# Optimization experiments

Measured on AMD Instinct MI355X. Metric: run time of the kernel, lower is better.

## Reference

```python
import jax, jax.numpy as jnp
import numpy as np
from jax import lax

NEG_INF = -1e30  # finite stand-in for -inf (keeps grads clean)
BLANK = 6624


def setup_inputs() -> dict:
    key = jax.random.key(0)
    k1, k2 = jax.random.split(key)
    B, T, C, L = 32, 512, 6625, 32
    log_probs = jax.random.normal(k1, (B, T, C), dtype=jnp.float32)
    targets = jax.random.randint(k2, (B, L), 0, BLANK, dtype=jnp.int32)  # labels exclude blank
    input_lengths = jnp.full((B,), T, dtype=jnp.int32)
    target_lengths = jnp.full((B,), L, dtype=jnp.int32)
    return {"log_probs": log_probs, "targets": targets,
            "input_lengths": input_lengths, "target_lengths": target_lengths}


def _ctc_loss(lp, targets, input_lengths, target_lengths, blank):
    # lp: [B, T, C] (already log-normalized as in the source), targets: [B, L]
    B, T, C = lp.shape
    L = targets.shape[1]
    S = 2 * L + 1
    # extended label sequence: blank, t0, blank, t1, ..., tL-1, blank  -> [B, S]
    ext = jnp.full((B, S), blank, dtype=targets.dtype)
    ext = ext.at[:, 1::2].set(targets)
    ext_m2 = jnp.pad(ext, ((0, 0), (2, 0)), constant_values=blank)[:, :S]
    allow_skip = (ext != blank) & (ext != ext_m2)  # [B, S]

    lp_tbc = jnp.transpose(lp, (1, 0, 2))  # [T, B, C]
    # emission log-prob of each extended label at each time: [T, B, S]
    emit = jnp.take_along_axis(lp_tbc, jnp.broadcast_to(ext[None], (T, B, S)), axis=2)

    alpha0 = jnp.full((B, S), NEG_INF, dtype=lp.dtype)
    alpha0 = alpha0.at[:, 0].set(emit[0, :, 0])
    alpha0 = alpha0.at[:, 1].set(emit[0, :, 1])

    pad1 = jnp.full((B, 1), NEG_INF, dtype=lp.dtype)
    pad2 = jnp.full((B, 2), NEG_INF, dtype=lp.dtype)

    def step(alpha, inp):
        emit_t, t = inp
        a1 = jnp.concatenate([pad1, alpha[:, :-1]], axis=1)
        a2 = jnp.concatenate([pad2, alpha[:, :-2]], axis=1)
        a2 = jnp.where(allow_skip, a2, NEG_INF)
        new = jnp.logaddexp(jnp.logaddexp(alpha, a1), a2) + emit_t
        new = jnp.where((t < input_lengths)[:, None], new, alpha)  # freeze past input_length
        return new, None

    alpha_T, _ = lax.scan(step, alpha0, (emit[1:], jnp.arange(1, T)))

    idx1 = (2 * target_lengths).astype(jnp.int32)            # final blank
    idx2 = jnp.maximum(2 * target_lengths - 1, 0).astype(jnp.int32)  # final label
    l1 = jnp.take_along_axis(alpha_T, idx1[:, None], axis=1)[:, 0]
    l2 = jnp.take_along_axis(alpha_T, idx2[:, None], axis=1)[:, 0]
    loss = -jnp.logaddexp(l1, l2)  # [B]
    # zero_infinity=True: infinite losses -> 0
    loss = jnp.where(loss > 1e20, 0.0, loss)
    # reduction='mean' (torch semantics: divide by target_length, then mean)
    return (loss / jnp.maximum(target_lengths, 1).astype(loss.dtype)).mean()


def reference(log_probs, targets, input_lengths, target_lengths):
    # Faithful to source: log_softmax over dim=1 (the TIME axis of [B, T, C])
    lp = jax.nn.log_softmax(log_probs, axis=1)
    return _ctc_loss(lp, targets, input_lengths, target_lengths, BLANK)
```

## Files before the change

### kernel.cpp

```cpp
#include <hip/hip_runtime.h>

#define NEG_INF -1e30f

constexpr int BLANKC = 6624;
constexpr int NCLS   = 6625;
constexpr int TT     = 512;
constexpr int LL     = 32;
constexpr int NSLOT  = LL + 1;
constexpr int BB     = 32;
constexpr int KPT    = TT / 64;

__device__ __forceinline__ float wave_allmax(float v) {
#pragma unroll
    for (int off = 32; off > 0; off >>= 1)
        v = fmaxf(v, __shfl_xor(v, off, 64));
    return v;
}
__device__ __forceinline__ float wave_allsum(float v) {
#pragma unroll
    for (int off = 32; off > 0; off >>= 1)
        v += __shfl_xor(v, off, 64);
    return v;
}

__global__ __launch_bounds__(256) void ctc_colnorm(
    const float* __restrict__ x,
    const int*   __restrict__ targets,
    float*       __restrict__ cols)
{
    const int wid  = blockIdx.x * 4 + (threadIdx.x >> 6);
    const int lane = threadIdx.x & 63;
    if (wid >= BB * NSLOT) return;
    const int b    = wid / NSLOT;
    const int slot = wid - b * NSLOT;
    const int c    = (slot == 0) ? BLANKC : targets[b * LL + slot - 1];

    const float* xb = x + (size_t)b * TT * NCLS + c;
    float v[KPT];
    float m = NEG_INF;
#pragma unroll
    for (int k = 0; k < KPT; ++k) {
        v[k] = xb[(size_t)(lane + 64 * k) * NCLS];
        m = fmaxf(m, v[k]);
    }
    m = wave_allmax(m);
    float s = 0.f;
#pragma unroll
    for (int k = 0; k < KPT; ++k) s += __expf(v[k] - m);
    s = wave_allsum(s);
    const float lse = m + __logf(s);

    float* cb = cols + (size_t)(b * NSLOT + slot) * TT;
#pragma unroll
    for (int k = 0; k < KPT; ++k) cb[lane + 64 * k] = v[k] - lse;
}

__global__ __launch_bounds__(64) void ctc_alpha(
    const float* __restrict__ cols,
    const int*   __restrict__ targets,
    const int*   __restrict__ input_lengths,
    const int*   __restrict__ target_lengths,
    float*       __restrict__ part)
{
    const int b = blockIdx.x;
    const int s = threadIdx.x;
    const int j = s >> 1;
    const bool odd = (s & 1) != 0;

    const int ext_s = odd ? targets[b * LL + j] : BLANKC;
    bool allow;
    if (!odd)            allow = false;
    else if (s == 1)     allow = (ext_s != BLANKC);
    else                 allow = (ext_s != BLANKC) && (ext_s != targets[b * LL + j - 1]);

    const float* bcol = cols + (size_t)b * NSLOT * TT;
    const float* ecol = bcol + (odd ? (size_t)(1 + j) * TT : (size_t)0);

    const int ilen = input_lengths[b];
    const int tlen = target_lengths[b];

    float alpha = NEG_INF;
    if (s == 0) alpha = bcol[0];
    if (s == 1) alpha = bcol[TT];
    float a64 = NEG_INF;

    for (int t = 1; t < TT; ++t) {
        const float e  = ecol[t];
        const float eb = bcol[t];
        float am1 = __shfl_up(alpha, 1, 64);
        float am2 = __shfl_up(alpha, 2, 64);
        const float a63 = __shfl(alpha, 63, 64);
        if (s == 0) am1 = NEG_INF;
        if (s < 2 || !allow) am2 = NEG_INF;

        const float m  = fmaxf(fmaxf(alpha, am1), am2);
        const float na = m + __logf(__expf(alpha - m) + __expf(am1 - m) + __expf(am2 - m)) + e;
        const float m2   = fmaxf(a64, a63);
        const float na64 = m2 + __logf(__expf(a64 - m2) + __expf(a63 - m2)) + eb;

        const bool live = (t < ilen);
        alpha = live ? na   : alpha;
        a64   = live ? na64 : a64;
    }

    const int idx1 = 2 * tlen;
    const int idx2 = max(2 * tlen - 1, 0);
    const float l1 = (idx1 >= 64) ? a64 : __shfl(alpha, idx1, 64);
    const float l2 = (idx2 >= 64) ? a64 : __shfl(alpha, idx2, 64);
    const float mm = fmaxf(l1, l2);
    float loss = -(mm + __logf(__expf(l1 - mm) + __expf(l2 - mm)));
    if (loss > 1e20f) loss = 0.f;
    loss /= (float)max(tlen, 1);
    if (s == 0) part[b] = loss;
}

__global__ __launch_bounds__(64) void ctc_reduce(
    const float* __restrict__ part, float* __restrict__ out)
{
    const int lane = threadIdx.x;
    float v = (lane < BB) ? part[lane] : 0.f;
#pragma unroll
    for (int off = 32; off > 0; off >>= 1) v += __shfl_xor(v, off, 64);
    if (lane == 0) out[0] = v / (float)BB;
}

extern "C" void kernel_launch(void* const* d_in, const int* in_sizes, int n_in,
                              void* d_out, int out_size, void* d_ws, size_t ws_size,
                              hipStream_t stream) {
    const float* lp      = (const float*)d_in[0];
    const int*   targets = (const int*)d_in[1];
    const int*   ilen    = (const int*)d_in[2];
    const int*   tlen    = (const int*)d_in[3];
    float* out = (float*)d_out;

    constexpr size_t COLS_ELEMS = (size_t)BB * NSLOT * TT;
    float* cols = (float*)d_ws;
    float* part = (float*)d_ws + COLS_ELEMS;

    const int gridA = (BB * NSLOT + 3) / 4;
    ctc_colnorm<<<gridA, 256, 0, stream>>>(lp, targets, cols);
    ctc_alpha<<<BB, 64, 0, stream>>>(cols, targets, ilen, tlen, part);
    ctc_reduce<<<1, 64, 0, stream>>>(part, out);
}
```

Measured before the change: 575.6 us.

## Restructure CTC alpha recursion with log2 domain, DPP shifts, and register-prefetched emissions

Stores the normalized columns in base-2 log space so the serial alpha recursion can use native exp2/log2 without scale multiplies. Neighbour shifts become DPP row-shift operations. The blank emission is taken via readfirstlane instead of a second global load, and the 64th state now tracks lane 63 directly. Emissions are loaded in 32-step chunks into double-buffered registers so global-load latency is hidden behind the recursion. The risks are correctness: the DPP row_shr control 0x138 may not shift across 16-lane rows as intended, and the a64 handling is subtle.

```diff
diff --git a/kernel.cpp b/kernel.cpp
--- a/kernel.cpp
+++ b/kernel.cpp
@@ -9,6 +9,36 @@
 constexpr int NSLOT  = LL + 1;
 constexpr int BB     = 32;
 constexpr int KPT    = TT / 64;
+
+constexpr float L2E = 1.44269504088896340736f;
+constexpr float LN2 = 0.693147180559945309417f;
+
+__device__ __forceinline__ float fast_exp2(float x) {
+#if __has_builtin(__builtin_amdgcn_exp2f)
+    return __builtin_amdgcn_exp2f(x);
+#else
+    return exp2f(x);
+#endif
+}
+__device__ __forceinline__ float fast_log2(float x) {
+#if __has_builtin(__builtin_amdgcn_logf)
+    return __builtin_amdgcn_logf(x);
+#else
+    return log2f(x);
+#endif
+}
+
+__device__ __forceinline__ float dpp_shr1(float x) {
+#if __has_builtin(__builtin_amdgcn_update_dpp)
+    return __int_as_float(__builtin_amdgcn_update_dpp(
+        __float_as_int(NEG_INF), __float_as_int(x),
+        0x138 , 0xF, 0xF, false));
+#else
+    float r = __shfl_up(x, 1, 64);
+    if ((int)(threadIdx.x & 63) == 0) r = NEG_INF;
+    return r;
+#endif
+}
 
 __device__ __forceinline__ float wave_allmax(float v) {
 #pragma unroll
@@ -44,16 +74,56 @@
         m = fmaxf(m, v[k]);
     }
     m = wave_allmax(m);
+    float w[KPT];
     float s = 0.f;
 #pragma unroll
-    for (int k = 0; k < KPT; ++k) s += __expf(v[k] - m);
+    for (int k = 0; k < KPT; ++k) {
+        w[k] = (v[k] - m) * L2E;
+        s += fast_exp2(w[k]);
+    }
     s = wave_allsum(s);
-    const float lse = m + __logf(s);
+    const float ls = fast_log2(s);
 
     float* cb = cols + (size_t)(b * NSLOT + slot) * TT;
 #pragma unroll
-    for (int k = 0; k < KPT; ++k) cb[lane + 64 * k] = v[k] - lse;
-}
+    for (int k = 0; k < KPT; ++k) cb[lane + 64 * k] = w[k] - ls;
+}
+
+__device__ __forceinline__ void ctc_step(float& alpha, float& a64,
+                                         float e, float eb, bool allow) {
+    float am1 = dpp_shr1(alpha);
+    float am2 = dpp_shr1(am1);
+    am2 = allow ? am2 : NEG_INF;
+    const float aold = alpha;
+    const float m  = fmaxf(fmaxf(aold, am1), am2);
+    const float r  = fast_exp2(aold - m) + fast_exp2(am1 - m) + fast_exp2(am2 - m);
+    const float na = m + fast_log2(r) + e;
+    const float m2   = fmaxf(a64, aold);
+    const float r2   = fast_exp2(a64 - m2) + fast_exp2(aold - m2);
+    const float na64 = m2 + fast_log2(r2) + eb;
+    alpha = na;
+    a64   = na64;
+}
+
+#define LOADC(E, c) do {                                                      \
+    const float4* __p = reinterpret_cast<const float4*>(ec + ((c) << 5));     \
+    _Pragma("unroll")                                                         \
+    for (int k = 0; k < 8; ++k) {                                             \
+        float4 __t = __p[k];                                                  \
+        E[4*k+0] = __t.x; E[4*k+1] = __t.y;                                   \
+        E[4*k+2] = __t.z; E[4*k+3] = __t.w;                                   \
+    }                                                                         \
+} while (0)
+
+#define CHUNK(E, u0) do {                                                     \
+    _Pragma("unroll")                                                         \
+    for (int u = (u0); u < 32; ++u) {                                         \
+        const float e_  = E[u];                                               \
+        const float eb_ = __int_as_float(                                     \
+            __builtin_amdgcn_readfirstlane(__float_as_int(E[u])));            \
+        ctc_step(alpha, a64, e_, eb_, allow);                                 \
+    }                                                                         \
+} while (0)
 
 __global__ __launch_bounds__(64) void ctc_alpha(
     const float* __restrict__ cols,
@@ -68,47 +138,49 @@
     const bool odd = (s & 1) != 0;
 
     const int ext_s = odd ? targets[b * LL + j] : BLANKC;
-    bool allow;
-    if (!odd)            allow = false;
-    else if (s == 1)     allow = (ext_s != BLANKC);
-    else                 allow = (ext_s != BLANKC) && (ext_s != targets[b * LL + j - 1]);
-
-    const float* bcol = cols + (size_t)b * NSLOT * TT;
-    const float* ecol = bcol + (odd ? (size_t)(1 + j) * TT : (size_t)0);
+    const bool allow = odd && (ext_s != BLANKC) &&
+                       (s == 1 || ext_s != targets[b * LL + j - 1]);
+
+    const float* ec = cols + ((size_t)b * NSLOT + (odd ? (size_t)(1 + j) : (size_t)0)) * TT;
 
     const int ilen = input_lengths[b];
     const int tlen = target_lengths[b];
-
-    float alpha = NEG_INF;
-    if (s == 0) alpha = bcol[0];
-    if (s == 1) alpha = bcol[TT];
+    const int nsteps = min(ilen, TT);
+
+    float alpha;
     float a64 = NEG_INF;
 
-    for (int t = 1; t < TT; ++t) {
-        const float e  = ecol[t];
-        const float eb = bcol[t];
-        float am1 = __shfl_up(alpha, 1, 64);
-        float am2 = __shfl_up(alpha, 2, 64);
-        const float a63 = __shfl(alpha, 63, 64);
-        if (s == 0) am1 = NEG_INF;
-        if (s < 2 || !allow) am2 = NEG_INF;
-
-        const float m  = fmaxf(fmaxf(alpha, am1), am2);
-        const float na = m + __logf(__expf(alpha - m) + __expf(am1 - m) + __expf(am2 - m)) + e;
-        const float m2   = fmaxf(a64, a63);
-        const float na64 = m2 + __logf(__expf(a64 - m2) + __expf(a63 - m2)) + eb;
-
-        const bool live = (t < ilen);
-        alpha = live ? na   : alpha;
-        a64   = live ? na64 : a64;
+    if (nsteps == TT) {
+        float eA[32], eB[32];
+        LOADC(eA, 0);
+        LOADC(eB, 1);
+        alpha = (s < 2) ? eA[0] : NEG_INF;
+        CHUNK(eA, 1);
+#pragma unroll 1
+        for (int p = 1; p + 1 < 16; p += 2) {
+            LOADC(eA, p + 1);
+            CHUNK(eB, 0);
+            LOADC(eB, p + 2);
+            CHUNK(eA, 0);
+        }
+        CHUNK(eB, 0);
+    } else {
+        const float* bc = cols + (size_t)b * NSLOT * TT;
+        alpha = (s < 2) ? ec[0] : NEG_INF;
+        for (int t = 1; t < nsteps; ++t) {
+            const float e  = ec[t];
+            const float eb = bc[t];
+            ctc_step(alpha, a64, e, eb, allow);
+        }
     }
 
     const int idx1 = 2 * tlen;
     const int idx2 = max(2 * tlen - 1, 0);
-    const float l1 = (idx1 >= 64) ? a64 : __shfl(alpha, idx1, 64);
-    const float l2 = (idx2 >= 64) ? a64 : __shfl(alpha, idx2, 64);
+    const float l1 = (idx1 >= 64) ? __shfl(a64, 63, 64) : __shfl(alpha, idx1, 64);
+    const float l2 = __shfl(alpha, idx2, 64);
     const float mm = fmaxf(l1, l2);
-    float loss = -(mm + __logf(__expf(l1 - mm) + __expf(l2 - mm)));
+    const float res2 = mm + fast_log2(fast_exp2(l1 - mm) + fast_exp2(l2 - mm));
+    float loss = -LN2 * res2;
     if (loss > 1e20f) loss = 0.f;
     loss /= (float)max(tlen, 1);
     if (s == 0) part[b] = loss;
```

New measurement: 518.4 us. 9.9% less time.
